# Kernel optimization log

Measured on AMD Instinct MI355X. Metric: run time of the kernel, lower is better.

## Reference

```python
import jax, jax.numpy as jnp
import numpy as np


@jax.custom_vjp
def spike(mem, v_th):
    # Heaviside forward, triangular surrogate backward (gamma=1.0)
    return (mem >= v_th).astype(mem.dtype)


def _spike_fwd(mem, v_th):
    return spike(mem, v_th), (mem, v_th)


def _spike_bwd(res, g):
    mem, v_th = res
    surr = jnp.clip(1.0 - jnp.abs(mem - v_th), 0.0)  # gamma = 1
    return (g * surr, jnp.zeros_like(v_th))  # torch returns None for threshold grad


spike.defvjp(_spike_fwd, _spike_bwd)


def setup_inputs() -> dict:
    key = jax.random.key(0)
    ks = jax.random.split(key, 6)
    T, B, C, H, W = 8, 16, 256, 32, 32
    NH, HID = 4, 64
    x = jax.random.normal(ks[0], (T, B, C, H, W), dtype=jnp.float32)
    decay_param = jnp.float32(np.log(0.85 / 0.15))  # logit(0.85)
    v_th = jnp.float32(0.5)
    W1 = jax.random.normal(ks[1], (NH, HID, T), dtype=jnp.float32) * 0.1
    b1 = jax.random.normal(ks[2], (NH, HID), dtype=jnp.float32) * 0.01
    W2 = jax.random.normal(ks[3], (NH, T, HID), dtype=jnp.float32) * 0.1
    b2 = jax.random.normal(ks[4], (NH, T), dtype=jnp.float32) * 0.01
    att_w = jnp.ones((NH,), dtype=jnp.float32) / NH
    return {"x": x, "decay_param": decay_param, "v_th": v_th,
            "W1": W1, "b1": b1, "W2": W2, "b2": b2, "att_w": att_w}


def reference(x, decay_param, v_th, W1, b1, W2, b2, att_w):
    T, B, C, H, W = x.shape
    d = jax.nn.sigmoid(decay_param)

    def step(carry, inp):
        mem, spk = carry  # detached states, as in the torch module
        m = d * (mem - v_th * spk) + inp
        denom = jnp.mean(jnp.abs(m), axis=(1, 2, 3), keepdims=True) + 1e-6
        m = m / denom
        s = spike(m, v_th)
        carry = (jax.lax.stop_gradient(m), jax.lax.stop_gradient(s))
        return carry, s

    init = (jnp.zeros_like(x[0]), jnp.zeros_like(x[0]))
    _, spikes = jax.lax.scan(step, init, x)          # [T,B,C,H,W]

    feats = spikes.reshape(T, B, C * H * W)          # [T,B,F]
    summary = feats.mean(axis=2).T                   # [B,T]
    # multi-head MLP attention over time
    h = jax.nn.relu(jnp.einsum('bt,nht->bnh', summary, W1) + b1[None])  # [B,NH,HID]
    maps = jnp.einsum('bnh,nth->bnt', h, W2) + b2[None]                  # [B,NH,T]
    weighted = jnp.sum(maps * att_w[None, :, None], axis=1)              # [B,T]
    aw = jax.nn.softmax(weighted, axis=-1).T[:, :, None]                 # [T,B,1]
    out = jnp.sum(feats * aw, axis=0)                                    # [B,F]
    return out
```

## Files before the change

kernel.cpp:

```cpp
#include <hip/hip_runtime.h>

#define NT    8
#define NB    16
#define FS    262144
#define TPB   256
#define BPB   64
#define GRID  (NB*BPB)
#define CHK   4
#define ELB   (TPB*CHK*4)
#define SPIN_CAP (1L<<26)

#define WS_SMALL 66624
#define WS_FAST  99392

__global__ __launch_bounds__(TPB, 4)
void bispike_kernel(const float* __restrict__ x,
                    const float* __restrict__ decay_p,
                    const float* __restrict__ vth_p,
                    const float* __restrict__ W1,
                    const float* __restrict__ b1,
                    const float* __restrict__ W2,
                    const float* __restrict__ b2,
                    const float* __restrict__ att_w,
                    float* __restrict__ out,
                    double* __restrict__ bsum,
                    int* __restrict__ scnt,
                    int* __restrict__ ccnt,
                    int* __restrict__ cnt,
                    int fastcnt)
{
    const int tid = threadIdx.x;
    const int b   = blockIdx.x / BPB;
    const int bg  = blockIdx.x % BPB;

    const double dec = 1.0 / (1.0 + exp(-(double)decay_p[0]));
    const double vth = (double)vth_p[0];

    double cv[CHK * 4];
    #pragma unroll
    for (int j = 0; j < CHK * 4; ++j) cv[j] = 0.0;
    float4 xv[CHK];
    unsigned sm[NT];

    {
        const float* p = x + (size_t)b * FS + (size_t)bg * ELB + tid * 4;
        #pragma unroll
        for (int k = 0; k < CHK; ++k) xv[k] = *(const float4*)(p + k * (TPB * 4));
    }

    __shared__ double dred[4];
    __shared__ double denom_s;

    #pragma unroll 1
    for (int t = 0; t < NT; ++t) {
        double lsum = 0.0;
        #pragma unroll
        for (int k = 0; k < CHK; ++k) {
            double m0 = dec * cv[k*4+0] + (double)xv[k].x;
            double m1 = dec * cv[k*4+1] + (double)xv[k].y;
            double m2 = dec * cv[k*4+2] + (double)xv[k].z;
            double m3 = dec * cv[k*4+3] + (double)xv[k].w;
            cv[k*4+0] = m0; cv[k*4+1] = m1; cv[k*4+2] = m2; cv[k*4+3] = m3;
            lsum += fabs(m0) + fabs(m1) + fabs(m2) + fabs(m3);
        }

        if (t < NT - 1) {
            const float* p = x + ((size_t)(t + 1) * NB + b) * FS
                               + (size_t)bg * ELB + tid * 4;
            #pragma unroll
            for (int k = 0; k < CHK; ++k) xv[k] = *(const float4*)(p + k * (TPB * 4));
        }

        #pragma unroll
        for (int off = 32; off > 0; off >>= 1)
            lsum += __shfl_down(lsum, off, 64);
        if ((tid & 63) == 0) dred[tid >> 6] = lsum;
        __syncthreads();

        if (tid < 64) {
            double bs = (dred[0] + dred[1]) + (dred[2] + dred[3]);
            double* slot = bsum + (size_t)(t * NB + b) * BPB;
            if (tid == 0)
                __hip_atomic_store(slot + bg, -bs,
                                   __ATOMIC_RELAXED, __HIP_MEMORY_SCOPE_AGENT);
            double v; long it = 0;
            for (;;) {
                v = __hip_atomic_load(slot + tid,
                                      __ATOMIC_RELAXED, __HIP_MEMORY_SCOPE_AGENT);
                if (__all(__double_as_longlong(v) != 0)) break;
                if (++it > SPIN_CAP) break;
                __builtin_amdgcn_s_sleep(1);
            }
            double tot = -v;
            #pragma unroll
            for (int off = 32; off > 0; off >>= 1)
                tot += __shfl_down(tot, off, 64);
            if (tid == 0)
                denom_s = tot / (double)FS + 1e-6;
        }
        __syncthreads();
        const double inv = 1.0 / denom_s;

        unsigned smt = 0;
        #pragma unroll
        for (int j = 0; j < CHK * 4; ++j) {
            double q = cv[j] * inv;
            if (q >= vth) { smt |= 1u << j; q -= vth; }
            cv[j] = q;
        }
        sm[t] = smt;
    }

    __shared__ int ired[NT][4];
    #pragma unroll
    for (int t = 0; t < NT; ++t) {
        int c = __popc(sm[t]);
        #pragma unroll
        for (int off = 32; off > 0; off >>= 1)
            c += __shfl_down(c, off, 64);
        if ((tid & 63) == 0) ired[t][tid >> 6] = c;
    }
    __syncthreads();

    __shared__ double summ_s[NT];
    __shared__ int totc_s[NT];

    if (fastcnt) {
        if (tid < 64) {
            int* cb = cnt + b * (NT * BPB);
            if (tid < NT) {
                int tot = (ired[tid][0] + ired[tid][1])
                        + (ired[tid][2] + ired[tid][3]);
                __hip_atomic_store(cb + tid * BPB + bg, tot + 1,
                                   __ATOMIC_RELAXED, __HIP_MEMORY_SCOPE_AGENT);
            }
            int vt[NT]; long it = 0;
            for (;;) {
                bool ok = true;
                #pragma unroll
                for (int t = 0; t < NT; ++t) {
                    vt[t] = __hip_atomic_load(cb + t * BPB + tid,
                                              __ATOMIC_RELAXED,
                                              __HIP_MEMORY_SCOPE_AGENT);
                    ok = ok && (vt[t] > 0);
                }
                if (__all(ok)) break;
                if (++it > SPIN_CAP) break;
                __builtin_amdgcn_s_sleep(1);
            }
            #pragma unroll
            for (int t = 0; t < NT; ++t) {
                int s = vt[t] - 1;
                #pragma unroll
                for (int off = 32; off > 0; off >>= 1)
                    s += __shfl_down(s, off, 64);
                if (tid == 0) totc_s[t] = s;
            }
        }
        __syncthreads();
        if (tid < NT)
            summ_s[tid] = (double)totc_s[tid] / (double)FS;
    } else {
        if (tid < NT) {
            int tot = (ired[tid][0] + ired[tid][1]) + (ired[tid][2] + ired[tid][3]);
            __hip_atomic_fetch_add(&scnt[tid * NB + b], tot,
                                   __ATOMIC_RELEASE, __HIP_MEMORY_SCOPE_AGENT);
        }
        __syncthreads();
        if (tid == 0) {
            __hip_atomic_fetch_add(&ccnt[b], 1,
                                   __ATOMIC_RELEASE, __HIP_MEMORY_SCOPE_AGENT);
            long it = 0;
            while (__hip_atomic_load(&ccnt[b], __ATOMIC_ACQUIRE,
                                     __HIP_MEMORY_SCOPE_AGENT) < BPB
                   && it++ < SPIN_CAP)
                __builtin_amdgcn_s_sleep(4);
        }
        __syncthreads();
        if (tid < NT) {
            int c = __hip_atomic_load(&scnt[tid * NB + b],
                                      __ATOMIC_ACQUIRE, __HIP_MEMORY_SCOPE_AGENT);
            summ_s[tid] = (double)c / (double)FS;
        }
    }
    __syncthreads();

    __shared__ double h_s[4 * 64];
    __shared__ double wmat_s[NT];
    {
        int nh = tid >> 6, hd = tid & 63;
        double acc = 0.0;
        #pragma unroll
        for (int t = 0; t < NT; ++t)
            acc += summ_s[t] * (double)W1[nh * 512 + hd * 8 + t];
        acc += (double)b1[nh * 64 + hd];
        h_s[tid] = fmax(acc, 0.0);
    }
    __syncthreads();
    if (tid < NT) {
        double w = 0.0;
        for (int nh = 0; nh < 4; ++nh) {
            double macc = 0.0;
            for (int hd = 0; hd < 64; ++hd)
                macc += h_s[nh * 64 + hd] * (double)W2[nh * 512 + tid * 64 + hd];
            macc += (double)b2[nh * 8 + tid];
            w += macc * (double)att_w[nh];
        }
        wmat_s[tid] = w;
    }
    __syncthreads();

    double awr[NT];
    {
        double mx = wmat_s[0];
        #pragma unroll
        for (int t = 1; t < NT; ++t) mx = fmax(mx, wmat_s[t]);
        double ss = 0.0;
        #pragma unroll
        for (int t = 0; t < NT; ++t) { awr[t] = exp(wmat_s[t] - mx); ss += awr[t]; }
        #pragma unroll
        for (int t = 0; t < NT; ++t) awr[t] = awr[t] / ss;
    }

    float* po = out + (size_t)b * FS + (size_t)bg * ELB + tid * 4;
    #pragma unroll
    for (int k = 0; k < CHK; ++k) {
        double o[4] = {0.0, 0.0, 0.0, 0.0};
        #pragma unroll
        for (int t = 0; t < NT; ++t) {
            const unsigned smt = sm[t];
            o[0] += ((smt >> (k * 4 + 0)) & 1) ? awr[t] : 0.0;
            o[1] += ((smt >> (k * 4 + 1)) & 1) ? awr[t] : 0.0;
            o[2] += ((smt >> (k * 4 + 2)) & 1) ? awr[t] : 0.0;
            o[3] += ((smt >> (k * 4 + 3)) & 1) ? awr[t] : 0.0;
        }
        *(float4*)(po + k * (TPB * 4)) =
            make_float4((float)o[0], (float)o[1], (float)o[2], (float)o[3]);
    }
}

__global__ void diag_kernel(float* out, int code) {
    out[0] = 100000.0f + (float)code;
}

extern "C" void kernel_launch(void* const* d_in, const int* in_sizes, int n_in,
                              void* d_out, int out_size, void* d_ws, size_t ws_size,
                              hipStream_t stream) {
    const float* x     = (const float*)d_in[0];
    const float* decay = (const float*)d_in[1];
    const float* vth   = (const float*)d_in[2];
    const float* W1    = (const float*)d_in[3];
    const float* b1    = (const float*)d_in[4];
    const float* W2    = (const float*)d_in[5];
    const float* b2    = (const float*)d_in[6];
    const float* att   = (const float*)d_in[7];
    float* out = (float*)d_out;

    if (ws_size < WS_SMALL) {
        diag_kernel<<<1, 1, 0, stream>>>(out, 999);
        return;
    }
    const int fastcnt = (ws_size >= (size_t)WS_FAST) ? 1 : 0;

    double* bsum = (double*)d_ws;
    int*    scnt = (int*)((char*)d_ws + 65536);
    int*    ccnt = (int*)((char*)d_ws + 66048);
    int*    cnt  = (int*)((char*)d_ws + 66624);

    hipMemsetAsync(d_ws, 0, fastcnt ? WS_FAST : WS_SMALL, stream);

    hipGetLastError();
    bispike_kernel<<<dim3(GRID), dim3(TPB), 0, stream>>>(
        x, decay, vth, W1, b1, W2, b2, att, out, bsum, scnt, ccnt, cnt, fastcnt);
    hipError_t err = hipGetLastError();
    if (err != hipSuccess) {
        diag_kernel<<<1, 1, 0, stream>>>(out, (int)err);
    }
}
```

Baseline: 244.0 us.

## Replace per-step block barriers with LDS flag spins and fuse normalization into recurrence

Removes the two __syncthreads per timestep. Each wave now publishes its partial abs-sum to LDS slots, wave 0 does the cross-block spin and posts the denominator through an LDS flag, and the other waves spin on that flag instead of waiting at a barrier. The membrane update is rewritten algebraically in unnormalized form: the threshold is scaled by the denominator and the divide is folded into the next step's fma, which saves one multiply pass per element and computes the next abs-sum in the same loop. The LDS spin-waits add s_sleep polling and depend on relaxed atomics staying visible, and the reordered floating-point arithmetic can flip spikes that sit near the threshold.

```diff
diff --git a/kernel.cpp b/kernel.cpp
--- a/kernel.cpp
+++ b/kernel.cpp
@@ -29,17 +29,24 @@
                     int* __restrict__ cnt,
                     int fastcnt)
 {
-    const int tid = threadIdx.x;
-    const int b   = blockIdx.x / BPB;
-    const int bg  = blockIdx.x % BPB;
-
-    const double dec = 1.0 / (1.0 + exp(-(double)decay_p[0]));
-    const double vth = (double)vth_p[0];
-
-    double cv[CHK * 4];
-    #pragma unroll
-    for (int j = 0; j < CHK * 4; ++j) cv[j] = 0.0;
-    float4 xv[CHK];
+    const int tid  = threadIdx.x;
+    const int lane = tid & 63;
+    const int wid  = tid >> 6;
+    const int b    = blockIdx.x / BPB;
+    const int bg   = blockIdx.x % BPB;
+
+    const double dec  = 1.0 / (1.0 + exp(-(double)decay_p[0]));
+    const double vth  = (double)vth_p[0];
+    const double csub = dec * vth;
+
+    __shared__ double wv[NT][4];
+    __shared__ double dn[NT];
+    if (tid < NT * 4) ((double*)wv)[tid] = 0.0;
+    if (tid < NT)     dn[tid] = 0.0;
+    __syncthreads();
+
+    double   u[CHK * 4];
+    float4   xv[CHK];
     unsigned sm[NT];
 
     {
@@ -47,23 +54,16 @@
         #pragma unroll
         for (int k = 0; k < CHK; ++k) xv[k] = *(const float4*)(p + k * (TPB * 4));
     }
-
-    __shared__ double dred[4];
-    __shared__ double denom_s;
+    double lsum = 0.0;
+    #pragma unroll
+    for (int k = 0; k < CHK; ++k) {
+        u[k*4+0] = (double)xv[k].x; u[k*4+1] = (double)xv[k].y;
+        u[k*4+2] = (double)xv[k].z; u[k*4+3] = (double)xv[k].w;
+        lsum += fabs(u[k*4+0]) + fabs(u[k*4+1]) + fabs(u[k*4+2]) + fabs(u[k*4+3]);
+    }
 
     #pragma unroll 1
     for (int t = 0; t < NT; ++t) {
-        double lsum = 0.0;
-        #pragma unroll
-        for (int k = 0; k < CHK; ++k) {
-            double m0 = dec * cv[k*4+0] + (double)xv[k].x;
-            double m1 = dec * cv[k*4+1] + (double)xv[k].y;
-            double m2 = dec * cv[k*4+2] + (double)xv[k].z;
-            double m3 = dec * cv[k*4+3] + (double)xv[k].w;
-            cv[k*4+0] = m0; cv[k*4+1] = m1; cv[k*4+2] = m2; cv[k*4+3] = m3;
-            lsum += fabs(m0) + fabs(m1) + fabs(m2) + fabs(m3);
-        }
-
         if (t < NT - 1) {
             const float* p = x + ((size_t)(t + 1) * NB + b) * FS
                                + (size_t)bg * ELB + tid * 4;
@@ -74,39 +74,84 @@
         #pragma unroll
         for (int off = 32; off > 0; off >>= 1)
             lsum += __shfl_down(lsum, off, 64);
-        if ((tid & 63) == 0) dred[tid >> 6] = lsum;
-        __syncthreads();
-
-        if (tid < 64) {
-            double bs = (dred[0] + dred[1]) + (dred[2] + dred[3]);
-            double* slot = bsum + (size_t)(t * NB + b) * BPB;
-            if (tid == 0)
-                __hip_atomic_store(slot + bg, -bs,
-                                   __ATOMIC_RELAXED, __HIP_MEMORY_SCOPE_AGENT);
-            double v; long it = 0;
+        if (lane == 0)
+            __hip_atomic_store(&wv[t][wid], -lsum, __ATOMIC_RELAXED,
+                               __HIP_MEMORY_SCOPE_WORKGROUP);
+
+        if (wid == 0) {
+            double w; long it = 0;
             for (;;) {
-                v = __hip_atomic_load(slot + tid,
-                                      __ATOMIC_RELAXED, __HIP_MEMORY_SCOPE_AGENT);
-                if (__all(__double_as_longlong(v) != 0)) break;
+                w = __hip_atomic_load(&wv[t][lane & 3], __ATOMIC_RELAXED,
+                                      __HIP_MEMORY_SCOPE_WORKGROUP);
+                if (__all(__double_as_longlong(w) != 0)) break;
                 if (++it > SPIN_CAP) break;
                 __builtin_amdgcn_s_sleep(1);
             }
-            double tot = -v;
+            w = -w;
+            w += __shfl_down(w, 2, 64);
+            w += __shfl_down(w, 1, 64);
+            const double blk = __shfl(w, 0, 64);
+
+            double* slot = bsum + (size_t)(t * NB + b) * BPB;
+            if (lane == 0)
+                __hip_atomic_store(slot + bg, -blk, __ATOMIC_RELAXED,
+                                   __HIP_MEMORY_SCOPE_AGENT);
+
+            double v = 0.0; it = 0;
+            for (;;) {
+                if (lane != bg)
+                    v = __hip_atomic_load(slot + lane, __ATOMIC_RELAXED,
+                                          __HIP_MEMORY_SCOPE_AGENT);
+                if (__all(lane == bg || __double_as_longlong(v) != 0)) break;
+                if (++it > SPIN_CAP) break;
+                __builtin_amdgcn_s_sleep(1);
+            }
+            double tot = (lane == bg) ? blk : -v;
             #pragma unroll
             for (int off = 32; off > 0; off >>= 1)
                 tot += __shfl_down(tot, off, 64);
-            if (tid == 0)
-                denom_s = tot / (double)FS + 1e-6;
-        }
-        __syncthreads();
-        const double inv = 1.0 / denom_s;
-
+            if (lane == 0)
+                __hip_atomic_store(&dn[t], tot / (double)FS + 1e-6,
+                                   __ATOMIC_RELAXED, __HIP_MEMORY_SCOPE_WORKGROUP);
+        }
+
+        double denom; long it2 = 0;
+        for (;;) {
+            denom = __hip_atomic_load(&dn[t], __ATOMIC_RELAXED,
+                                      __HIP_MEMORY_SCOPE_WORKGROUP);
+            if (__double_as_longlong(denom) != 0) break;
+            if (++it2 > SPIN_CAP) break;
+            __builtin_amdgcn_s_sleep(1);
+        }
+
+        const double thr = vth * denom;
+        const double a   = dec * (1.0 / denom);
         unsigned smt = 0;
-        #pragma unroll
-        for (int j = 0; j < CHK * 4; ++j) {
-            double q = cv[j] * inv;
-            if (q >= vth) { smt |= 1u << j; q -= vth; }
-            cv[j] = q;
+        if (t < NT - 1) {
+            double nl = 0.0;
+            #pragma unroll
+            for (int k = 0; k < CHK; ++k) {
+                const double xn0 = (double)xv[k].x, xn1 = (double)xv[k].y,
+                             xn2 = (double)xv[k].z, xn3 = (double)xv[k].w;
+                double un;
+                bool s0 = (u[k*4+0] >= thr); if (s0) smt |= 1u << (k*4+0);
+                un = fma(a, u[k*4+0], xn0); if (s0) un -= csub;
+                u[k*4+0] = un; nl += fabs(un);
+                bool s1 = (u[k*4+1] >= thr); if (s1) smt |= 1u << (k*4+1);
+                un = fma(a, u[k*4+1], xn1); if (s1) un -= csub;
+                u[k*4+1] = un; nl += fabs(un);
+                bool s2 = (u[k*4+2] >= thr); if (s2) smt |= 1u << (k*4+2);
+                un = fma(a, u[k*4+2], xn2); if (s2) un -= csub;
+                u[k*4+2] = un; nl += fabs(un);
+                bool s3 = (u[k*4+3] >= thr); if (s3) smt |= 1u << (k*4+3);
+                un = fma(a, u[k*4+3], xn3); if (s3) un -= csub;
+                u[k*4+3] = un; nl += fabs(un);
+            }
+            lsum = nl;
+        } else {
+            #pragma unroll
+            for (int j = 0; j < CHK * 4; ++j)
+                if (u[j] >= thr) smt |= 1u << j;
         }
         sm[t] = smt;
     }
@@ -118,7 +163,7 @@
         #pragma unroll
         for (int off = 32; off > 0; off >>= 1)
             c += __shfl_down(c, off, 64);
-        if ((tid & 63) == 0) ired[t][tid >> 6] = c;
+        if (lane == 0) ired[t][wid] = c;
     }
     __syncthreads();
 
```

New measurement: 249.5 us. +2.2%, slower.
